# Optimization experiments

Hardware: AMD Instinct MI355X
Metric: run time of the kernel (lower is better)

## Reference

```python
import jax, jax.numpy as jnp
import numpy as np

NUM_BANDS = 64
LATENT = 256
HIDDEN = 512
G = 8
K = 1024
GD = LATENT // G  # 32
BETA = 0.25


def setup_inputs() -> dict:
    key = jax.random.key(0)
    ks = jax.random.split(key, 10)
    B, T = 16, 1000
    bands = jax.random.normal(ks[0], (B, T, NUM_BANDS), dtype=jnp.float32)
    s = 0.02
    enc_w1 = jax.random.normal(ks[1], (NUM_BANDS, HIDDEN), dtype=jnp.float32) * s
    enc_b1 = jnp.zeros((HIDDEN,), dtype=jnp.float32)
    enc_w2 = jax.random.normal(ks[2], (HIDDEN, LATENT), dtype=jnp.float32) * s
    enc_b2 = jnp.zeros((LATENT,), dtype=jnp.float32)
    codebooks = jax.random.normal(ks[3], (G, K, GD), dtype=jnp.float32) * 0.1
    dec_w1 = jax.random.normal(ks[4], (LATENT, HIDDEN), dtype=jnp.float32) * s
    dec_b1 = jnp.zeros((HIDDEN,), dtype=jnp.float32)
    dec_w2 = jax.random.normal(ks[5], (HIDDEN, NUM_BANDS), dtype=jnp.float32) * s
    dec_b2 = jnp.zeros((NUM_BANDS,), dtype=jnp.float32)
    return {
        "bands": bands,
        "enc_w1": enc_w1, "enc_b1": enc_b1, "enc_w2": enc_w2, "enc_b2": enc_b2,
        "codebooks": codebooks,
        "dec_w1": dec_w1, "dec_b1": dec_b1, "dec_w2": dec_w2, "dec_b2": dec_b2,
    }


def _mlp(x, w1, b1, w2, b2):
    # TimeDistributedMLP: Linear -> ReLU -> Linear applied on last dim
    return jax.nn.relu(x @ w1 + b1) @ w2 + b2


def reference(bands, enc_w1, enc_b1, enc_w2, enc_b2, codebooks,
              dec_w1, dec_b1, dec_w2, dec_b2):
    B, T, _ = bands.shape
    z_e = _mlp(bands, enc_w1, enc_b1, enc_w2, enc_b2)  # (B,T,LATENT)

    # Grouped VQ over flattened frames
    parts = z_e.reshape(B * T, G, GD)                   # (N,G,gd)
    zn = jnp.sum(parts * parts, axis=-1)[:, :, None]    # (N,G,1)
    cn = jnp.sum(codebooks * codebooks, axis=-1)[None]  # (1,G,K)
    cross = jnp.einsum('ngd,gkd->ngk', parts, codebooks)
    dist = zn - 2.0 * cross + cn                        # (N,G,K)
    idx = jnp.argmin(dist, axis=-1)                     # (N,G) int
    z_q = codebooks[jnp.arange(G)[None, :], idx]        # (N,G,gd) gather

    # straight-through estimator
    z_q_st = parts + jax.lax.stop_gradient(z_q - parts)

    # per-group mean losses, summed over groups
    codebook_loss = jnp.sum(jnp.mean((jax.lax.stop_gradient(z_q) - parts) ** 2, axis=(0, 2)))
    commit_loss = jnp.sum(jnp.mean((z_q - jax.lax.stop_gradient(parts)) ** 2, axis=(0, 2)))
    vq_loss = BETA * (codebook_loss + commit_loss)  # epoch=None -> beta_eff = beta

    z_q_out = z_q_st.reshape(B, T, LATENT)
    idx_out = idx.reshape(B, T, G)
    bands_hat = _mlp(z_q_out, dec_w1, dec_b1, dec_w2, dec_b2)
    return (bands_hat, z_e, z_q_out, idx_out, vq_loss)
```

## Files before the change

kernel.cpp:

```cpp
#include <hip/hip_runtime.h>

#define NBANDS 64
#define LATENT 256
#define HIDDEN 512
#define GQ 8
#define KQ 1024
#define GD 32
#define NROWS 16000

#define OUT_BH   0
#define OUT_ZE   1024000
#define OUT_ZQ   5120000
#define OUT_IDX  9216000
#define OUT_LOSS 9344000

#define WS_H     0
#define WS_H2BF_F  0
#define WS_ZQB_F   4096000
#define WS_W1B_F   6144000
#define WS_W2B_F   6209536
#define WS_CN    8192000
#define WS_LOSS  8200192

typedef __attribute__((ext_vector_type(8))) short bf16x8;
typedef __attribute__((ext_vector_type(4))) float f32x4;

__device__ __forceinline__ unsigned short f2bf(float f) {
  unsigned u = __builtin_bit_cast(unsigned, f);
  unsigned r = u + 0x7FFFu + ((u >> 16) & 1u);
  return (unsigned short)(r >> 16);
}

template<int BN, int TM, int TN, bool RELU>
__global__ __launch_bounds__(256) void gemm_f32(
    const float* __restrict__ A, const float* __restrict__ B,
    const float* __restrict__ bias, float* __restrict__ C,
    int M, int N, int K) {
  constexpr int BM = 128;
  constexpr int BK = 16;
  constexpr int NTX = BN / TN;

  __shared__ float As[BK][BM + 8];
  __shared__ float Bs[BK][BN + 4];

  const int tid = threadIdx.x;
  const int tx = tid % NTX;
  const int ty = tid / NTX;
  const int row0 = blockIdx.y * BM;
  const int col0 = blockIdx.x * BN;

  const int arow = tid >> 1;
  const int akq  = (tid & 1) * 8;
  const int bkk = tid >> 4;
  const int bn  = (tid & 15) * (BN / 16);

  float acc[TM][TN] = {};

  for (int k0 = 0; k0 < K; k0 += BK) {
    float4 av0 = *reinterpret_cast<const float4*>(
        &A[(size_t)(row0 + arow) * K + k0 + akq]);
    float4 av1 = *reinterpret_cast<const float4*>(
        &A[(size_t)(row0 + arow) * K + k0 + akq + 4]);
    float4 bv0, bv1;
    bv0 = *reinterpret_cast<const float4*>(
        &B[(size_t)(k0 + bkk) * N + col0 + bn]);
    if (BN == 128)
      bv1 = *reinterpret_cast<const float4*>(
          &B[(size_t)(k0 + bkk) * N + col0 + bn + 4]);
    __syncthreads();
    As[akq + 0][arow] = av0.x; As[akq + 1][arow] = av0.y;
    As[akq + 2][arow] = av0.z; As[akq + 3][arow] = av0.w;
    As[akq + 4][arow] = av1.x; As[akq + 5][arow] = av1.y;
    As[akq + 6][arow] = av1.z; As[akq + 7][arow] = av1.w;
    *reinterpret_cast<float4*>(&Bs[bkk][bn]) = bv0;
    if (BN == 128)
      *reinterpret_cast<float4*>(&Bs[bkk][bn + 4]) = bv1;
    __syncthreads();

#pragma unroll
    for (int kk = 0; kk < BK; ++kk) {
      float a[TM], b[TN];
#pragma unroll
      for (int q = 0; q < TM / 4; ++q) {
        float4 v = *reinterpret_cast<const float4*>(&As[kk][ty * TM + q * 4]);
        a[q * 4 + 0] = v.x; a[q * 4 + 1] = v.y;
        a[q * 4 + 2] = v.z; a[q * 4 + 3] = v.w;
      }
#pragma unroll
      for (int q = 0; q < TN / 4; ++q) {
        float4 v = *reinterpret_cast<const float4*>(&Bs[kk][tx * TN + q * 4]);
        b[q * 4 + 0] = v.x; b[q * 4 + 1] = v.y;
        b[q * 4 + 2] = v.z; b[q * 4 + 3] = v.w;
      }
#pragma unroll
      for (int i = 0; i < TM; ++i)
#pragma unroll
        for (int j = 0; j < TN; ++j)
          acc[i][j] = fmaf(a[i], b[j], acc[i][j]);
    }
  }

  float bb[TN];
#pragma unroll
  for (int q = 0; q < TN / 4; ++q) {
    float4 v = *reinterpret_cast<const float4*>(&bias[col0 + tx * TN + q * 4]);
    bb[q * 4 + 0] = v.x; bb[q * 4 + 1] = v.y;
    bb[q * 4 + 2] = v.z; bb[q * 4 + 3] = v.w;
  }
#pragma unroll
  for (int i = 0; i < TM; ++i) {
    const int r = row0 + ty * TM + i;
#pragma unroll
    for (int q = 0; q < TN / 4; ++q) {
      float4 v;
      float* vp = &v.x;
#pragma unroll
      for (int j = 0; j < 4; ++j) {
        float t = acc[i][q * 4 + j] + bb[q * 4 + j];
        if (RELU) t = fmaxf(t, 0.0f);
        vp[j] = t;
      }
      *reinterpret_cast<float4*>(&C[(size_t)r * N + col0 + tx * TN + q * 4]) = v;
    }
  }
}

template<int WM, bool OUT_BF16>
__global__ __launch_bounds__(256) void gemm_bf16_mfma(
    const unsigned short* __restrict__ A, const unsigned short* __restrict__ B,
    const float* __restrict__ bias, void* __restrict__ Cout,
    int M, int N, int K) {
  constexpr int BM = 4 * WM;
  constexpr int MT = WM / 16;

  __shared__ unsigned short As[BM][40];
  __shared__ unsigned short Bs[64][40];

  const int tid  = threadIdx.x;
  const int wave = tid >> 6;
  const int lane = tid & 63;
  const int quad = lane >> 4;
  const int l16  = lane & 15;
  const int row0 = blockIdx.y * BM;
  const int col0 = blockIdx.x * 64;

  f32x4 acc[MT][4];
#pragma unroll
  for (int mt = 0; mt < MT; ++mt)
#pragma unroll
    for (int nt = 0; nt < 4; ++nt) acc[mt][nt] = (f32x4){0.f, 0.f, 0.f, 0.f};

  for (int k0 = 0; k0 < K; k0 += 32) {
    __syncthreads();
    if constexpr (BM == 128) {
      const int r = tid >> 1, seg = (tid & 1) * 16;
      const uint4* src = reinterpret_cast<const uint4*>(
          &A[(size_t)(row0 + r) * K + k0 + seg]);
      uint4* dst = reinterpret_cast<uint4*>(&As[r][seg]);
      dst[0] = src[0]; dst[1] = src[1];
    } else {
      const int r = tid >> 2, seg = (tid & 3) * 8;
      *reinterpret_cast<uint4*>(&As[r][seg]) =
          *reinterpret_cast<const uint4*>(&A[(size_t)(row0 + r) * K + k0 + seg]);
    }
    {
      const int kk = tid >> 3, n0 = (tid & 7) * 8;
      uint4 bv = *reinterpret_cast<const uint4*>(
          &B[(size_t)(k0 + kk) * N + col0 + n0]);
      unsigned short t[8];
      *reinterpret_cast<uint4*>(t) = bv;
#pragma unroll
      for (int j = 0; j < 8; ++j) Bs[n0 + j][kk] = t[j];
    }
    __syncthreads();

    bf16x8 af[MT], bf[4];
#pragma unroll
    for (int mt = 0; mt < MT; ++mt)
      af[mt] = *reinterpret_cast<const bf16x8*>(
          &As[wave * WM + mt * 16 + l16][quad * 8]);
#pragma unroll
    for (int nt = 0; nt < 4; ++nt)
      bf[nt] = *reinterpret_cast<const bf16x8*>(&Bs[nt * 16 + l16][quad * 8]);
#pragma unroll
    for (int mt = 0; mt < MT; ++mt)
#pragma unroll
      for (int nt = 0; nt < 4; ++nt)
        acc[mt][nt] = __builtin_amdgcn_mfma_f32_16x16x32_bf16(
            af[mt], bf[nt], acc[mt][nt], 0, 0, 0);
  }

#pragma unroll
  for (int mt = 0; mt < MT; ++mt)
#pragma unroll
    for (int nt = 0; nt < 4; ++nt) {
      const int col = col0 + nt * 16 + l16;
      const float bv = bias[col];
#pragma unroll
      for (int r = 0; r < 4; ++r) {
        const int grow = row0 + wave * WM + mt * 16 + quad * 4 + r;
        float v = acc[mt][nt][r] + bv;
        if constexpr (OUT_BF16) {
          v = fmaxf(v, 0.0f);
          ((unsigned short*)Cout)[(size_t)grow * N + col] = f2bf(v);
        } else {
          ((float*)Cout)[(size_t)grow * N + col] = v;
        }
      }
    }
}

__global__ void cn_kernel(const float* __restrict__ cb, float* __restrict__ cn,
                          float* __restrict__ loss_acc) {
  const int i = blockIdx.x * 256 + threadIdx.x;
  if (i == 0) loss_acc[0] = 0.0f;
  if (i < GQ * KQ) {
    const float* c = cb + (size_t)i * GD;
    float s = 0.0f;
#pragma unroll
    for (int d = 0; d < GD; ++d) s = fmaf(c[d], c[d], s);
    cn[i] = s;
  }
}

__global__ void wconv_kernel(const float* __restrict__ w1, const float* __restrict__ w2,
                             unsigned short* __restrict__ w1b,
                             unsigned short* __restrict__ w2b) {
  const int i = blockIdx.x * 256 + threadIdx.x;
  const int n1 = LATENT * HIDDEN;
  const int n2 = HIDDEN * NBANDS;
  if (i < n1) w1b[i] = f2bf(w1[i]);
  else if (i < n1 + n2) w2b[i - n1] = f2bf(w2[i - n1]);
}

#define VQ_ROWS 128
#define VQ_CHUNK 128
#define VQ_NCHUNK (KQ / VQ_CHUNK)
#define ZPAD 36
#define MPAD 129

__global__ __launch_bounds__(256) void vq_kernel(
    const float* __restrict__ z_e, const float* __restrict__ cb,
    const float* __restrict__ cn, float* __restrict__ z_q,
    unsigned short* __restrict__ zqb,
    float* __restrict__ idx_out, float* __restrict__ loss_acc) {
  const int g    = blockIdx.y;
  const int row0 = blockIdx.x * VQ_ROWS;
  const int tid  = threadIdx.x;
  const int tx   = tid & 15;
  const int ty   = tid >> 4;

  __shared__ float z_lds[VQ_ROWS][ZPAD];
  __shared__ float cb_lds[VQ_CHUNK][ZPAD];
  __shared__ float cn_lds[VQ_CHUNK];

  const float* cbg = cb + (size_t)g * KQ * GD;
  const float* cng = cn + (size_t)g * KQ;

  {
    const int r   = tid >> 1;
    const int off = (tid & 1) << 4;
    const float4* src = reinterpret_cast<const float4*>(
        &z_e[(size_t)(row0 + r) * LATENT + g * GD + off]);
#pragma unroll
    for (int q = 0; q < 4; ++q)
      *reinterpret_cast<float4*>(&z_lds[r][off + q * 4]) = src[q];
  }

  float best[8];
  int   bidx[8];
#pragma unroll
  for (int i = 0; i < 8; ++i) { best[i] = 3.0e38f; bidx[i] = 0; }

  for (int ch = 0; ch < VQ_NCHUNK; ++ch) {
    __syncthreads();
    {
      const int kc  = tid >> 1;
      const int off = (tid & 1) << 4;
      const float4* src = reinterpret_cast<const float4*>(
          &cbg[(size_t)(ch * VQ_CHUNK + kc) * GD + off]);
#pragma unroll
      for (int q = 0; q < 4; ++q)
        *reinterpret_cast<float4*>(&cb_lds[kc][off + q * 4]) = src[q];
      if (tid < VQ_CHUNK) cn_lds[tid] = cng[ch * VQ_CHUNK + tid];
    }
    __syncthreads();

    float acc[8][8];
#pragma unroll
    for (int i = 0; i < 8; ++i)
#pragma unroll
      for (int j = 0; j < 8; ++j) acc[i][j] = 0.0f;

#pragma unroll 2
    for (int d0 = 0; d0 < GD; d0 += 4) {
      float4 a[8], b[8];
#pragma unroll
      for (int i = 0; i < 8; ++i)
        a[i] = *reinterpret_cast<const float4*>(&z_lds[ty * 8 + i][d0]);
#pragma unroll
      for (int j = 0; j < 8; ++j)
        b[j] = *reinterpret_cast<const float4*>(&cb_lds[j * 16 + tx][d0]);
#pragma unroll
      for (int i = 0; i < 8; ++i)
#pragma unroll
        for (int j = 0; j < 8; ++j) {
          float t = acc[i][j];
          t = fmaf(a[i].x, b[j].x, t);
          t = fmaf(a[i].y, b[j].y, t);
          t = fmaf(a[i].z, b[j].z, t);
          t = fmaf(a[i].w, b[j].w, t);
          acc[i][j] = t;
        }
    }

#pragma unroll
    for (int j = 0; j < 8; ++j) {
      const float cnv = cn_lds[j * 16 + tx];
      const int k = ch * VQ_CHUNK + j * 16 + tx;
#pragma unroll
      for (int i = 0; i < 8; ++i) {
        const float dist = fmaf(-2.0f, acc[i][j], cnv);
        if (dist < best[i]) { best[i] = dist; bidx[i] = k; }
      }
    }
  }

  __syncthreads();
  float* m_d = &cb_lds[0][0];
  int*   m_i = reinterpret_cast<int*>(&cb_lds[0][0]) + 16 * MPAD + 16;
#pragma unroll
  for (int i = 0; i < 8; ++i) {
    m_d[tx * MPAD + ty * 8 + i] = best[i];
    m_i[tx * MPAD + ty * 8 + i] = bidx[i];
  }
  __syncthreads();

  float sse_part = 0.0f;
  if (tid < VQ_ROWS) {
    const int row = tid;
    float mb = m_d[row];
    int   mi = m_i[row];
#pragma unroll
    for (int t = 1; t < 16; ++t) {
      const float v = m_d[t * MPAD + row];
      const int  ix = m_i[t * MPAD + row];
      if (v < mb || (v == mb && ix < mi)) { mb = v; mi = ix; }
    }

    const float* c = cbg + (size_t)mi * GD;
    float cw[GD];
#pragma unroll
    for (int q = 0; q < 8; ++q) {
      float4 v = *reinterpret_cast<const float4*>(&c[q * 4]);
      cw[q * 4 + 0] = v.x; cw[q * 4 + 1] = v.y;
      cw[q * 4 + 2] = v.z; cw[q * 4 + 3] = v.w;
    }
    float sse = 0.0f;
#pragma unroll
    for (int d = 0; d < GD; ++d) {
      const float diff = cw[d] - z_lds[row][d];
      sse = fmaf(diff, diff, sse);
    }
    float4* zq = reinterpret_cast<float4*>(
        &z_q[(size_t)(row0 + row) * LATENT + g * GD]);
#pragma unroll
    for (int q = 0; q < 8; ++q)
      zq[q] = make_float4(cw[q * 4], cw[q * 4 + 1], cw[q * 4 + 2], cw[q * 4 + 3]);

    alignas(16) unsigned short zb[GD];
#pragma unroll
    for (int d = 0; d < GD; ++d) zb[d] = f2bf(cw[d]);
    uint4* dstb = reinterpret_cast<uint4*>(
        zqb + (size_t)(row0 + row) * LATENT + g * GD);
    const uint4* srcb = reinterpret_cast<const uint4*>(zb);
#pragma unroll
    for (int q = 0; q < 4; ++q) dstb[q] = srcb[q];

    idx_out[(size_t)(row0 + row) * GQ + g] = (float)mi;
    sse_part = sse;
  }

  __syncthreads();
  if (tid < VQ_ROWS) cn_lds[tid] = sse_part;
  __syncthreads();
  if (tid < 64) {
    float s = cn_lds[tid] + cn_lds[tid + 64];
#pragma unroll
    for (int off = 32; off > 0; off >>= 1)
      s += __shfl_down(s, off, 64);
    if (tid == 0) atomicAdd(loss_acc, s);
  }
}

__global__ void loss_kernel(const float* __restrict__ acc,
                            float* __restrict__ out) {
  out[0] = 0.5f * acc[0] / (float)((size_t)NROWS * GD);
}

extern "C" void kernel_launch(void* const* d_in, const int* in_sizes, int n_in,
                              void* d_out, int out_size, void* d_ws, size_t ws_size,
                              hipStream_t stream) {
  const float* bands  = (const float*)d_in[0];
  const float* enc_w1 = (const float*)d_in[1];
  const float* enc_b1 = (const float*)d_in[2];
  const float* enc_w2 = (const float*)d_in[3];
  const float* enc_b2 = (const float*)d_in[4];
  const float* cbooks = (const float*)d_in[5];
  const float* dec_w1 = (const float*)d_in[6];
  const float* dec_b1 = (const float*)d_in[7];
  const float* dec_w2 = (const float*)d_in[8];
  const float* dec_b2 = (const float*)d_in[9];

  float* out = (float*)d_out;
  float* ws  = (float*)d_ws;

  float* bands_hat = out + OUT_BH;
  float* z_e       = out + OUT_ZE;
  float* z_q       = out + OUT_ZQ;
  float* idx_f     = out + OUT_IDX;
  float* loss_out  = out + OUT_LOSS;

  float* H        = ws + WS_H;
  float* cn       = ws + WS_CN;
  float* loss_acc = ws + WS_LOSS;
  unsigned short* h2bf = (unsigned short*)(ws + WS_H2BF_F);
  unsigned short* zqb  = (unsigned short*)(ws + WS_ZQB_F);
  unsigned short* w1b  = (unsigned short*)(ws + WS_W1B_F);
  unsigned short* w2b  = (unsigned short*)(ws + WS_W2B_F);

  cn_kernel<<<dim3((GQ * KQ + 255) / 256), dim3(256), 0, stream>>>(cbooks, cn, loss_acc);

  gemm_f32<128, 8, 8, true ><<<dim3(HIDDEN / 128, NROWS / 128), dim3(256), 0, stream>>>(
      bands, enc_w1, enc_b1, H, NROWS, HIDDEN, NBANDS);
  gemm_f32<64, 4, 8, false><<<dim3(LATENT / 64, NROWS / 128), dim3(256), 0, stream>>>(
      H, enc_w2, enc_b2, z_e, NROWS, LATENT, HIDDEN);

  wconv_kernel<<<dim3((LATENT * HIDDEN + HIDDEN * NBANDS + 255) / 256), dim3(256), 0, stream>>>(
      dec_w1, dec_w2, w1b, w2b);

  vq_kernel<<<dim3(NROWS / VQ_ROWS, GQ), dim3(256), 0, stream>>>(
      z_e, cbooks, cn, z_q, zqb, idx_f, loss_acc);

  gemm_bf16_mfma<32, true ><<<dim3(HIDDEN / 64, NROWS / 128), dim3(256), 0, stream>>>(
      zqb, w1b, dec_b1, (void*)h2bf, NROWS, HIDDEN, LATENT);
  gemm_bf16_mfma<16, false><<<dim3(NBANDS / 64, NROWS / 64), dim3(256), 0, stream>>>(
      h2bf, w2b, dec_b2, (void*)bands_hat, NROWS, NBANDS, HIDDEN);

  loss_kernel<<<1, 1, 0, stream>>>(loss_acc, loss_out);
}
```

Baseline: 322.5 us.

## Read VQ codebook directly from global memory instead of staging in LDS

The VQ kernel no longer stages each 128-entry codebook chunk and its norms in shared memory. Each thread now loads its codebook rows and norms straight from global memory, relying on cache since the codebook is shared by all blocks. This removes two barriers per chunk. The z row reads from LDS are rotated by ty, apparently to reduce bank conflicts. The cost is more global/L1 traffic in the inner loop, with float4 loads strided by GD across threads, which may coalesce poorly.

```diff
diff --git a/kernel.cpp b/kernel.cpp
--- a/kernel.cpp
+++ b/kernel.cpp
@@ -237,7 +237,6 @@
 #define VQ_CHUNK 128
 #define VQ_NCHUNK (KQ / VQ_CHUNK)
 #define ZPAD 36
-#define MPAD 129
 
 __global__ __launch_bounds__(256) void vq_kernel(
     const float* __restrict__ z_e, const float* __restrict__ cb,
@@ -251,10 +250,12 @@
   const int ty   = tid >> 4;
 
   __shared__ float z_lds[VQ_ROWS][ZPAD];
-  __shared__ float cb_lds[VQ_CHUNK][ZPAD];
-  __shared__ float cn_lds[VQ_CHUNK];
+  __shared__ float m_d[16][129];
+  __shared__ int   m_i[16][129];
+  __shared__ float red[VQ_ROWS];
 
   const float* cbg = cb + (size_t)g * KQ * GD;
+  const float* cbt = cbg + (size_t)tx * GD;
   const float* cng = cn + (size_t)g * KQ;
 
   {
@@ -266,6 +267,7 @@
     for (int q = 0; q < 4; ++q)
       *reinterpret_cast<float4*>(&z_lds[r][off + q * 4]) = src[q];
   }
+  __syncthreads();
 
   float best[8];
   int   bidx[8];
@@ -273,34 +275,25 @@
   for (int i = 0; i < 8; ++i) { best[i] = 3.0e38f; bidx[i] = 0; }
 
   for (int ch = 0; ch < VQ_NCHUNK; ++ch) {
-    __syncthreads();
-    {
-      const int kc  = tid >> 1;
-      const int off = (tid & 1) << 4;
-      const float4* src = reinterpret_cast<const float4*>(
-          &cbg[(size_t)(ch * VQ_CHUNK + kc) * GD + off]);
-#pragma unroll
-      for (int q = 0; q < 4; ++q)
-        *reinterpret_cast<float4*>(&cb_lds[kc][off + q * 4]) = src[q];
-      if (tid < VQ_CHUNK) cn_lds[tid] = cng[ch * VQ_CHUNK + tid];
-    }
-    __syncthreads();
-
     float acc[8][8];
 #pragma unroll
     for (int i = 0; i < 8; ++i)
 #pragma unroll
       for (int j = 0; j < 8; ++j) acc[i][j] = 0.0f;
+
+    const float* cbc = cbt + (size_t)ch * VQ_CHUNK * GD;
 
 #pragma unroll 2
     for (int d0 = 0; d0 < GD; d0 += 4) {
       float4 a[8], b[8];
 #pragma unroll
-      for (int i = 0; i < 8; ++i)
+      for (int s = 0; s < 8; ++s) {
+        const int i = (s + ty) & 7;
         a[i] = *reinterpret_cast<const float4*>(&z_lds[ty * 8 + i][d0]);
+      }
 #pragma unroll
       for (int j = 0; j < 8; ++j)
-        b[j] = *reinterpret_cast<const float4*>(&cb_lds[j * 16 + tx][d0]);
+        b[j] = *reinterpret_cast<const float4*>(&cbc[j * 16 * GD + d0]);
 #pragma unroll
       for (int i = 0; i < 8; ++i)
 #pragma unroll
@@ -316,8 +309,8 @@
 
 #pragma unroll
     for (int j = 0; j < 8; ++j) {
-      const float cnv = cn_lds[j * 16 + tx];
       const int k = ch * VQ_CHUNK + j * 16 + tx;
+      const float cnv = cng[k];
 #pragma unroll
       for (int i = 0; i < 8; ++i) {
         const float dist = fmaf(-2.0f, acc[i][j], cnv);
@@ -326,25 +319,22 @@
     }
   }
 
-  __syncthreads();
-  float* m_d = &cb_lds[0][0];
-  int*   m_i = reinterpret_cast<int*>(&cb_lds[0][0]) + 16 * MPAD + 16;
 #pragma unroll
   for (int i = 0; i < 8; ++i) {
-    m_d[tx * MPAD + ty * 8 + i] = best[i];
-    m_i[tx * MPAD + ty * 8 + i] = bidx[i];
+    m_d[tx][ty * 8 + i] = best[i];
+    m_i[tx][ty * 8 + i] = bidx[i];
   }
   __syncthreads();
 
   float sse_part = 0.0f;
   if (tid < VQ_ROWS) {
     const int row = tid;
-    float mb = m_d[row];
-    int   mi = m_i[row];
+    float mb = m_d[0][row];
+    int   mi = m_i[0][row];
 #pragma unroll
     for (int t = 1; t < 16; ++t) {
-      const float v = m_d[t * MPAD + row];
-      const int  ix = m_i[t * MPAD + row];
+      const float v = m_d[t][row];
+      const int  ix = m_i[t][row];
       if (v < mb || (v == mb && ix < mi)) { mb = v; mi = ix; }
     }
 
@@ -381,11 +371,10 @@
     sse_part = sse;
   }
 
-  __syncthreads();
-  if (tid < VQ_ROWS) cn_lds[tid] = sse_part;
+  if (tid < VQ_ROWS) red[tid] = sse_part;
   __syncthreads();
   if (tid < 64) {
-    float s = cn_lds[tid] + cn_lds[tid + 64];
+    float s = red[tid] + red[tid + 64];
 #pragma unroll
     for (int off = 32; off > 0; off >>= 1)
       s += __shfl_down(s, off, 64);
```

Measured after the change: 773.7 us. +139.9%, slower.
